# Performance work log

Hardware: AMD Instinct MI355X
Metric: run time of the kernel (lower is better)

The kernel has to match this reference:

```python
import jax, jax.numpy as jnp
import numpy as np

DIM = 512

def setup_inputs() -> dict:
    key = jax.random.key(0)
    kx, kq, kk, kv = jax.random.split(key, 4)
    x = jax.random.normal(kx, (8, 2048, DIM), dtype=jnp.float32)
    # Dense kernels are [in_dim, out_dim], no bias
    Wq = jax.random.normal(kq, (DIM, DIM), dtype=jnp.float32) * (DIM ** -0.5)
    Wk = jax.random.normal(kk, (DIM, DIM), dtype=jnp.float32) * (DIM ** -0.5)
    Wv = jax.random.normal(kv, (DIM, DIM), dtype=jnp.float32) * (DIM ** -0.5)
    return {"x": x, "Wq": Wq, "Wk": Wk, "Wv": Wv}

def reference(x, Wq, Wk, Wv):
    # x: [b, s, d]
    q = jnp.einsum('bsd,de->bse', x, Wq)
    k = jnp.einsum('bsd,de->bse', x, Wk)
    v = jnp.einsum('bsd,de->bse', x, Wv)
    scale = jnp.sqrt(jnp.asarray(DIM, dtype=x.dtype))
    attn = jnp.einsum('bqe,bke->bqk', q, k) / scale  # [b, s, s]
    attn = jax.nn.softmax(attn, axis=-1)
    return jnp.einsum('bqk,bke->bqe', attn, v)  # [b, s, d]
```

## Files before the change

kernel.cpp:

```cpp
#include <hip/hip_runtime.h>
#include <stdint.h>

typedef unsigned short u16;
typedef unsigned int u32;
typedef float floatx4 __attribute__((ext_vector_type(4)));
typedef __bf16 bf16x8 __attribute__((ext_vector_type(8)));
typedef __attribute__((address_space(1))) const u32 gu32;
typedef __attribute__((address_space(3))) u32 lu32;

#define SEQ 2048
#define DIM 512
#define NBATCH 8

#if defined(__has_builtin)
#if __has_builtin(__builtin_amdgcn_cvt_pk_bf16_f32)
#define HAVE_PK_BF16 1
#endif
#endif
#ifndef HAVE_PK_BF16
#define HAVE_PK_BF16 0
#endif

__device__ __forceinline__ u16 f2bf(float f) {
#if HAVE_PK_BF16
  auto p = __builtin_amdgcn_cvt_pk_bf16_f32(f, f);
  union { decltype(p) v; u16 u[2]; } cv; cv.v = p;
  return cv.u[0];
#else
  u32 u = __float_as_uint(f);
  u += 0x7fffu + ((u >> 16) & 1u);
  return (u16)(u >> 16);
#endif
}

__device__ __forceinline__ void stage_tile64(const u16* __restrict__ g, int ld, int k0, u16* lds) {
  const int t = threadIdx.x;
  const int wave = t >> 6, lane = t & 63;
  const int rsub = lane >> 3;
  const int lg = (lane & 7) ^ rsub;
#pragma unroll
  for (int q = 0; q < 4; ++q) {
    const int chunk = wave * 4 + q;
    const int row = chunk * 8 + rsub;
    const u16* gp = g + (size_t)row * ld + k0 + lg * 8;
    u16* lp = lds + chunk * 512 + lane * 8;
    __builtin_amdgcn_global_load_lds((gu32*)gp, (lu32*)lp, 16, 0, 0);
  }
}

__device__ __forceinline__ void gemm_core(const u16* A, const u16* BT, int lda, int ldb, int kdim,
                                          u16* As, u16* Bs, floatx4 acc[4][4]) {
  const int t = threadIdx.x;
  const int wave = t >> 6, lane = t & 63;
  const int wr = (wave >> 1) * 64, wc = (wave & 1) * 64;
  const int l15 = lane & 15, quad = lane >> 4;
  const int swz = l15 & 7;
  for (int k0 = 0; k0 < kdim; k0 += 64) {
    stage_tile64(A, lda, k0, As);
    stage_tile64(BT, ldb, k0, Bs);
    __syncthreads();
#pragma unroll
    for (int ks = 0; ks < 2; ++ks) {
      const int pg = ((ks << 2) + quad) ^ swz;
      bf16x8 af[4], bfr[4];
#pragma unroll
      for (int i = 0; i < 4; ++i) {
        af[i]  = *(const bf16x8*)(As + (wr + i * 16 + l15) * 64 + pg * 8);
        bfr[i] = *(const bf16x8*)(Bs + (wc + i * 16 + l15) * 64 + pg * 8);
      }
#pragma unroll
      for (int mi = 0; mi < 4; ++mi)
#pragma unroll
        for (int ni = 0; ni < 4; ++ni)
          acc[mi][ni] = __builtin_amdgcn_mfma_f32_16x16x32_bf16(af[mi], bfr[ni], acc[mi][ni], 0, 0, 0);
    }
    __syncthreads();
  }
}

__device__ __forceinline__ void zero_acc(floatx4 acc[4][4]) {
#pragma unroll
  for (int i = 0; i < 4; ++i)
#pragma unroll
    for (int j = 0; j < 4; ++j)
      acc[i][j] = (floatx4){0.f, 0.f, 0.f, 0.f};
}

__global__ __launch_bounds__(256) void k_prep(const float* __restrict__ x,
                                              const float* __restrict__ Wq, const float* __restrict__ Wk,
                                              const float* __restrict__ Wv,
                                              u16* __restrict__ xb, u16* __restrict__ wt) {
  __shared__ float tile[64][65];
  const int t = threadIdx.x;
  if (blockIdx.x < 4096) {
    size_t i = ((size_t)blockIdx.x * 256 + t) * 8;
    float4 a = *(const float4*)(x + i);
    float4 b = *(const float4*)(x + i + 4);
    u16 o[8] = {f2bf(a.x), f2bf(a.y), f2bf(a.z), f2bf(a.w),
                f2bf(b.x), f2bf(b.y), f2bf(b.z), f2bf(b.w)};
    *(uint4*)(xb + i) = *(const uint4*)o;
    return;
  }
  const int r = blockIdx.x - 4096;
  const int sec = r >> 6, rem = r & 63;
  const int kb = (rem & 7) * 64, nb0 = (rem >> 3) * 64;
  const float* W = (sec == 0) ? Wq : (sec == 1) ? Wk : Wv;
#pragma unroll
  for (int i = 0; i < 4; ++i) {
    int kr = i * 16 + (t >> 4), nc = (t & 15) * 4;
    float4 v = *(const float4*)&W[(size_t)(kb + kr) * 512 + nb0 + nc];
    tile[kr][nc] = v.x; tile[kr][nc + 1] = v.y; tile[kr][nc + 2] = v.z; tile[kr][nc + 3] = v.w;
  }
  __syncthreads();
#pragma unroll
  for (int i = 0; i < 4; ++i) {
    int nr = i * 16 + (t >> 4), kc = (t & 15) * 4;
    u16 o[4] = {f2bf(tile[kc][nr]), f2bf(tile[kc + 1][nr]), f2bf(tile[kc + 2][nr]), f2bf(tile[kc + 3][nr])};
    *(uint2*)&wt[(size_t)(sec * 512 + nb0 + nr) * 512 + kb + kc] = *(const uint2*)o;
  }
}

__global__ __launch_bounds__(256, 4) void k_qkv(const u16* __restrict__ xb, const u16* __restrict__ wt,
                                                u16* __restrict__ qo, u16* __restrict__ ko,
                                                u16* __restrict__ vt) {
  __shared__ __align__(16) u16 As[128 * 64];
  __shared__ __align__(16) u16 Bs[128 * 64];
  const int m0 = blockIdx.x * 128, n0 = blockIdx.y * 128;
  floatx4 acc[4][4];
  zero_acc(acc);
  gemm_core(xb + (size_t)m0 * DIM, wt + (size_t)n0 * DIM, DIM, DIM, DIM, As, Bs, acc);
  const int t = threadIdx.x, wave = t >> 6, lane = t & 63;
  const int wr = (wave >> 1) * 64, wc = (wave & 1) * 64;
  const int l15 = lane & 15, quad = lane >> 4;
  const int sec = n0 >> 9;
#pragma unroll
  for (int mi = 0; mi < 4; ++mi)
#pragma unroll
    for (int ni = 0; ni < 4; ++ni)
#pragma unroll
      for (int r = 0; r < 4; ++r) {
        int m = m0 + wr + mi * 16 + quad * 4 + r;
        int n = n0 + wc + ni * 16 + l15;
        float v = acc[mi][ni][r];
        int nc = n & 511;
        if (sec == 0) {
          qo[(size_t)m * DIM + nc] = f2bf(v * 0.04419417382415922f);
        } else if (sec == 1) {
          ko[(size_t)m * DIM + nc] = f2bf(v);
        } else {
          int b = m >> 11, s = m & 2047;
          vt[((size_t)(b * DIM + nc)) * SEQ + s] = f2bf(v);
        }
      }
}

__global__ __launch_bounds__(256, 4) void k_scores(const u16* __restrict__ q, const u16* __restrict__ kk,
                                                   u16* __restrict__ sc, float* __restrict__ rowsum,
                                                   int b0) {
  __shared__ __align__(16) u16 As[128 * 64];
  __shared__ __align__(16) u16 Bs[128 * 64];
  const int bz = blockIdx.z, bb = b0 + bz;
  const int xcd = blockIdx.x & 7, j = blockIdx.x >> 3;
  const int m0 = (j & 15) * 128, n0 = (xcd * 2 + (j >> 4)) * 128;
  floatx4 acc[4][4];
  zero_acc(acc);
  gemm_core(q + (size_t)bb * SEQ * DIM + (size_t)m0 * DIM,
            kk + (size_t)bb * SEQ * DIM + (size_t)n0 * DIM, DIM, DIM, DIM, As, Bs, acc);
  u16* C = sc + (size_t)bz * SEQ * SEQ;
  float* rsb = rowsum + (size_t)bb * SEQ;
  const int t = threadIdx.x, wave = t >> 6, lane = t & 63;
  const int wr = (wave >> 1) * 64, wc = (wave & 1) * 64;
  const int l15 = lane & 15, quad = lane >> 4;
#pragma unroll
  for (int mi = 0; mi < 4; ++mi)
#pragma unroll
    for (int r = 0; r < 4; ++r) {
      int m = m0 + wr + mi * 16 + quad * 4 + r;
      float p = 0.f;
      float ev[4];
#pragma unroll
      for (int ni = 0; ni < 4; ++ni) {
        ev[ni] = __expf(acc[mi][ni][r]);
        p += ev[ni];
      }
#pragma unroll
      for (int ni = 0; ni < 4; ++ni) {
        int n = n0 + wc + ni * 16 + l15;
        C[(size_t)m * SEQ + n] = f2bf(ev[ni]);
      }
      p += __shfl_xor(p, 1); p += __shfl_xor(p, 2);
      p += __shfl_xor(p, 4); p += __shfl_xor(p, 8);
      if (l15 == 0) atomicAdd(&rsb[m], p);
    }
}

__global__ __launch_bounds__(256, 4) void k_pv(const u16* __restrict__ sc, const u16* __restrict__ vt,
                                               const float* __restrict__ rowsum,
                                               float* __restrict__ out, int b0) {
  __shared__ __align__(16) u16 As[128 * 64];
  __shared__ __align__(16) u16 Bs[128 * 64];
  const int bz = blockIdx.z, bb = b0 + bz;
  const int xcd = blockIdx.x & 7, j = blockIdx.x >> 3;
  const int m0 = (xcd * 2 + (j & 1)) * 128, n0 = (j >> 1) * 128;
  floatx4 acc[4][4];
  zero_acc(acc);
  gemm_core(sc + (size_t)bz * SEQ * SEQ + (size_t)m0 * SEQ,
            vt + (size_t)bb * DIM * SEQ + (size_t)n0 * SEQ, SEQ, SEQ, SEQ, As, Bs, acc);
  float* C = out + (size_t)bb * SEQ * DIM;
  const float* rsb = rowsum + (size_t)bb * SEQ;
  const int t = threadIdx.x, wave = t >> 6, lane = t & 63;
  const int wr = (wave >> 1) * 64, wc = (wave & 1) * 64;
  const int l15 = lane & 15, quad = lane >> 4;
#pragma unroll
  for (int mi = 0; mi < 4; ++mi)
#pragma unroll
    for (int r = 0; r < 4; ++r) {
      int m = m0 + wr + mi * 16 + quad * 4 + r;
      float inv = 1.0f / rsb[m];
#pragma unroll
      for (int ni = 0; ni < 4; ++ni) {
        int n = n0 + wc + ni * 16 + l15;
        C[(size_t)m * DIM + n] = acc[mi][ni][r] * inv;
      }
    }
}

extern "C" void kernel_launch(void* const* d_in, const int* in_sizes, int n_in,
                              void* d_out, int out_size, void* d_ws, size_t ws_size,
                              hipStream_t stream) {
  const float* x  = (const float*)d_in[0];
  const float* Wq = (const float*)d_in[1];
  const float* Wk = (const float*)d_in[2];
  const float* Wv = (const float*)d_in[3];
  float* out = (float*)d_out;
  char* ws = (char*)d_ws;

  u16* xb   = (u16*)(ws + 0);
  u16* wt   = (u16*)(ws + 16777216);
  u16* qo   = (u16*)(ws + 18350080);
  u16* ko   = (u16*)(ws + 35127296);
  u16* vt   = (u16*)(ws + 51904512);
  float* rs = (float*)(ws + 68681728);
  u16* sc   = (u16*)(ws + 68747264);
  const size_t base_need = 68747264;
  const size_t per_b = (size_t)SEQ * SEQ * 2;
  size_t avail = (ws_size > base_need) ? (ws_size - base_need) : 0;
  int nb = (int)(avail / per_b);
  if (nb < 1) nb = 1;
  if (nb > NBATCH) nb = NBATCH;

  hipMemsetAsync(rs, 0, (size_t)NBATCH * SEQ * sizeof(float), stream);
  k_prep<<<dim3(4288), dim3(256), 0, stream>>>(x, Wq, Wk, Wv, xb, wt);
  k_qkv<<<dim3(128, 12), dim3(256), 0, stream>>>(xb, wt, qo, ko, vt);
  for (int b0 = 0; b0 < NBATCH; b0 += nb) {
    int nbr = (NBATCH - b0 < nb) ? (NBATCH - b0) : nb;
    k_scores<<<dim3(256, 1, nbr), dim3(256), 0, stream>>>(qo, ko, sc, rs, b0);
    k_pv<<<dim3(64, 1, nbr), dim3(256), 0, stream>>>(sc, vt, rs, out, b0);
  }
}
```

Measured before the change: 216.3 us.

## Double-buffer LDS staging in GEMM core and compute V^T with a separate GEMM

The shared GEMM core now double-buffers its LDS tiles, issuing the async global-to-LDS loads for the next K tile before computing the current one, and drops one barrier per iteration. The aim is to overlap memory fetches with MFMA work. V is now produced by a dedicated kernel that computes W_v^T·x^T directly, so V^T is written with coalesced rows instead of the earlier strided transposed stores. The trade-off is twice the LDS per block, which can lower occupancy below the four blocks per CU the launch bounds request.

```diff
diff --git a/kernel.cpp b/kernel.cpp
--- a/kernel.cpp
+++ b/kernel.cpp
@@ -11,6 +11,7 @@
 #define SEQ 2048
 #define DIM 512
 #define NBATCH 8
+#define TOTS (NBATCH * SEQ)
 
 #if defined(__has_builtin)
 #if __has_builtin(__builtin_amdgcn_cvt_pk_bf16_f32)
@@ -55,18 +56,26 @@
   const int wr = (wave >> 1) * 64, wc = (wave & 1) * 64;
   const int l15 = lane & 15, quad = lane >> 4;
   const int swz = l15 & 7;
+  stage_tile64(A, lda, 0, As);
+  stage_tile64(BT, ldb, 0, Bs);
+  __syncthreads();
+  int cur = 0;
   for (int k0 = 0; k0 < kdim; k0 += 64) {
-    stage_tile64(A, lda, k0, As);
-    stage_tile64(BT, ldb, k0, Bs);
-    __syncthreads();
+    const int lastiter = (k0 + 64 >= kdim);
+    if (!lastiter) {
+      stage_tile64(A, lda, k0 + 64, As + ((cur ^ 1) * (128 * 64)));
+      stage_tile64(BT, ldb, k0 + 64, Bs + ((cur ^ 1) * (128 * 64)));
+    }
+    const u16* Ac = As + cur * (128 * 64);
+    const u16* Bc = Bs + cur * (128 * 64);
 #pragma unroll
     for (int ks = 0; ks < 2; ++ks) {
       const int pg = ((ks << 2) + quad) ^ swz;
       bf16x8 af[4], bfr[4];
 #pragma unroll
       for (int i = 0; i < 4; ++i) {
-        af[i]  = *(const bf16x8*)(As + (wr + i * 16 + l15) * 64 + pg * 8);
-        bfr[i] = *(const bf16x8*)(Bs + (wc + i * 16 + l15) * 64 + pg * 8);
+        af[i]  = *(const bf16x8*)(Ac + (wr + i * 16 + l15) * 64 + pg * 8);
+        bfr[i] = *(const bf16x8*)(Bc + (wc + i * 16 + l15) * 64 + pg * 8);
       }
 #pragma unroll
       for (int mi = 0; mi < 4; ++mi)
@@ -74,7 +83,8 @@
         for (int ni = 0; ni < 4; ++ni)
           acc[mi][ni] = __builtin_amdgcn_mfma_f32_16x16x32_bf16(af[mi], bfr[ni], acc[mi][ni], 0, 0, 0);
     }
-    __syncthreads();
+    if (!lastiter) __syncthreads();
+    cur ^= 1;
   }
 }
 
@@ -121,10 +131,9 @@
 }
 
 __global__ __launch_bounds__(256, 4) void k_qkv(const u16* __restrict__ xb, const u16* __restrict__ wt,
-                                                u16* __restrict__ qo, u16* __restrict__ ko,
-                                                u16* __restrict__ vt) {
-  __shared__ __align__(16) u16 As[128 * 64];
-  __shared__ __align__(16) u16 Bs[128 * 64];
+                                                u16* __restrict__ qo, u16* __restrict__ ko) {
+  __shared__ __align__(16) u16 As[2 * 128 * 64];
+  __shared__ __align__(16) u16 Bs[2 * 128 * 64];
   const int m0 = blockIdx.x * 128, n0 = blockIdx.y * 128;
   floatx4 acc[4][4];
   zero_acc(acc);
@@ -133,6 +142,32 @@
   const int wr = (wave >> 1) * 64, wc = (wave & 1) * 64;
   const int l15 = lane & 15, quad = lane >> 4;
   const int sec = n0 >> 9;
+  u16* __restrict__ C = sec ? ko : qo;
+  const float scl = sec ? 1.0f : 0.04419417382415922f;
+#pragma unroll
+  for (int mi = 0; mi < 4; ++mi)
+#pragma unroll
+    for (int ni = 0; ni < 4; ++ni)
+#pragma unroll
+      for (int r = 0; r < 4; ++r) {
+        int m = m0 + wr + mi * 16 + quad * 4 + r;
+        int nc = (n0 + wc + ni * 16 + l15) & 511;
+        C[(size_t)m * DIM + nc] = f2bf(acc[mi][ni][r] * scl);
+      }
+}
+
+__global__ __launch_bounds__(256, 4) void k_vt(const u16* __restrict__ xb, const u16* __restrict__ wt,
+                                               u16* __restrict__ vt) {
+  __shared__ __align__(16) u16 As[2 * 128 * 64];
+  __shared__ __align__(16) u16 Bs[2 * 128 * 64];
+  const int m0 = blockIdx.x * 128;
+  const int n0 = blockIdx.y * 128;
+  floatx4 acc[4][4];
+  zero_acc(acc);
+  gemm_core(wt + (size_t)(2 * DIM + m0) * DIM, xb + (size_t)n0 * DIM, DIM, DIM, DIM, As, Bs, acc);
+  const int t = threadIdx.x, wave = t >> 6, lane = t & 63;
+  const int wr = (wave >> 1) * 64, wc = (wave & 1) * 64;
+  const int l15 = lane & 15, quad = lane >> 4;
 #pragma unroll
   for (int mi = 0; mi < 4; ++mi)
 #pragma unroll
@@ -141,24 +176,15 @@
       for (int r = 0; r < 4; ++r) {
         int m = m0 + wr + mi * 16 + quad * 4 + r;
         int n = n0 + wc + ni * 16 + l15;
-        float v = acc[mi][ni][r];
-        int nc = n & 511;
-        if (sec == 0) {
-          qo[(size_t)m * DIM + nc] = f2bf(v * 0.04419417382415922f);
-        } else if (sec == 1) {
-          ko[(size_t)m * DIM + nc] = f2bf(v);
-        } else {
-          int b = m >> 11, s = m & 2047;
-          vt[((size_t)(b * DIM + nc)) * SEQ + s] = f2bf(v);
-        }
+        vt[(size_t)m * TOTS + n] = f2bf(acc[mi][ni][r]);
       }
 }
 
 __global__ __launch_bounds__(256, 4) void k_scores(const u16* __restrict__ q, const u16* __restrict__ kk,
                                                    u16* __restrict__ sc, float* __restrict__ rowsum,
                                                    int b0) {
-  __shared__ __align__(16) u16 As[128 * 64];
-  __shared__ __align__(16) u16 Bs[128 * 64];
+  __shared__ __align__(16) u16 As[2 * 128 * 64];
+  __shared__ __align__(16) u16 Bs[2 * 128 * 64];
   const int bz = blockIdx.z, bb = b0 + bz;
   const int xcd = blockIdx.x & 7, j = blockIdx.x >> 3;
   const int m0 = (j & 15) * 128, n0 = (xcd * 2 + (j >> 4)) * 128;
@@ -197,15 +223,15 @@
 __global__ __launch_bounds__(256, 4) void k_pv(const u16* __restrict__ sc, const u16* __restrict__ vt,
                                                const float* __restrict__ rowsum,
                                                float* __restrict__ out, int b0) {
-  __shared__ __align__(16) u16 As[128 * 64];
-  __shared__ __align__(16) u16 Bs[128 * 64];
+  __shared__ __align__(16) u16 As[2 * 128 * 64];
+  __shared__ __align__(16) u16 Bs[2 * 128 * 64];
   const int bz = blockIdx.z, bb = b0 + bz;
   const int xcd = blockIdx.x & 7, j = blockIdx.x >> 3;
   const int m0 = (xcd * 2 + (j & 1)) * 128, n0 = (j >> 1) * 128;
   floatx4 acc[4][4];
   zero_acc(acc);
   gemm_core(sc + (size_t)bz * SEQ * SEQ + (size_t)m0 * SEQ,
-            vt + (size_t)bb * DIM * SEQ + (size_t)n0 * SEQ, SEQ, SEQ, SEQ, As, Bs, acc);
+            vt + (size_t)n0 * TOTS + (size_t)bb * SEQ, SEQ, TOTS, SEQ, As, Bs, acc);
   float* C = out + (size_t)bb * SEQ * DIM;
   const float* rsb = rowsum + (size_t)bb * SEQ;
   const int t = threadIdx.x, wave = t >> 6, lane = t & 63;
@@ -251,7 +277,8 @@
 
   hipMemsetAsync(rs, 0, (size_t)NBATCH * SEQ * sizeof(float), stream);
   k_prep<<<dim3(4288), dim3(256), 0, stream>>>(x, Wq, Wk, Wv, xb, wt);
-  k_qkv<<<dim3(128, 12), dim3(256), 0, stream>>>(xb, wt, qo, ko, vt);
+  k_qkv<<<dim3(128, 8), dim3(256), 0, stream>>>(xb, wt, qo, ko);
+  k_vt<<<dim3(4, 128), dim3(256), 0, stream>>>(xb, wt, vt);
   for (int b0 = 0; b0 < NBATCH; b0 += nb) {
     int nbr = (NBATCH - b0 < nb) ? (NBATCH - b0) : nb;
     k_scores<<<dim3(256, 1, nbr), dim3(256), 0, stream>>>(qo, ko, sc, rs, b0);
```

Result: slower. 229.7 us (+6.2%).

## Use 3-stage LDS ring pipeline with 256x128 tiles and 8-wave blocks

Applied to the files above, without the earlier changes.

Replaces the synchronous stage-then-compute GEMM loop with a three-slot LDS ring that prefetches two k-steps ahead using vmcnt waits and a single barrier per step. Blocks grow to 512 threads covering 256x128 output tiles, which halves the grid sizes. The V projection is recomputed as a transposed GEMM (W^T times x) so V^T is written with coalesced stores instead of strided scatter. This is meant to hide global-load latency and improve operand reuse, at the cost of much larger LDS use per block (144 KB), fewer resident blocks and fewer blocks to fill the CUs.

```diff
diff --git a/kernel.cpp b/kernel.cpp
--- a/kernel.cpp
+++ b/kernel.cpp
@@ -11,6 +11,7 @@
 #define SEQ 2048
 #define DIM 512
 #define NBATCH 8
+#define TOTS (NBATCH * SEQ)
 
 #if defined(__has_builtin)
 #if __has_builtin(__builtin_amdgcn_cvt_pk_bf16_f32)
@@ -33,7 +34,8 @@
 #endif
 }
 
-__device__ __forceinline__ void stage_tile64(const u16* __restrict__ g, int ld, int k0, u16* lds) {
+
+__device__ __forceinline__ void stageA(const u16* __restrict__ g, int ld, int k0, u16* lds) {
   const int t = threadIdx.x;
   const int wave = t >> 6, lane = t & 63;
   const int rsub = lane >> 3;
@@ -48,25 +50,55 @@
   }
 }
 
-__device__ __forceinline__ void gemm_core(const u16* A, const u16* BT, int lda, int ldb, int kdim,
+__device__ __forceinline__ void stageB(const u16* __restrict__ g, int ld, int k0, u16* lds) {
+  const int t = threadIdx.x;
+  const int wave = t >> 6, lane = t & 63;
+  const int rsub = lane >> 3;
+  const int lg = (lane & 7) ^ rsub;
+#pragma unroll
+  for (int q = 0; q < 2; ++q) {
+    const int chunk = wave * 2 + q;
+    const int row = chunk * 8 + rsub;
+    const u16* gp = g + (size_t)row * ld + k0 + lg * 8;
+    u16* lp = lds + chunk * 512 + lane * 8;
+    __builtin_amdgcn_global_load_lds((gu32*)gp, (lu32*)lp, 16, 0, 0);
+  }
+}
+
+__device__ __forceinline__ void gemm_ring(const u16* __restrict__ A, int lda,
+                                          const u16* __restrict__ BT, int ldb, int kdim,
                                           u16* As, u16* Bs, floatx4 acc[4][4]) {
   const int t = threadIdx.x;
-  const int wave = t >> 6, lane = t & 63;
-  const int wr = (wave >> 1) * 64, wc = (wave & 1) * 64;
+  const int w = t >> 6, lane = t & 63;
+  const int wm = w & 3, wn = w >> 2;
   const int l15 = lane & 15, quad = lane >> 4;
   const int swz = l15 & 7;
-  for (int k0 = 0; k0 < kdim; k0 += 64) {
-    stage_tile64(A, lda, k0, As);
-    stage_tile64(BT, ldb, k0, Bs);
-    __syncthreads();
+  const int nsteps = kdim >> 6;
+
+  stageA(A, lda, 0, As);           stageB(BT, ldb, 0, Bs);
+  stageA(A, lda, 64, As + 16384);  stageB(BT, ldb, 64, Bs + 8192);
+
+  int slot = 0;
+  for (int kt = 0; kt < nsteps; ++kt) {
+    if (kt + 1 < nsteps) asm volatile("s_waitcnt vmcnt(6)" ::: "memory");
+    else                 asm volatile("s_waitcnt vmcnt(0)" ::: "memory");
+    __builtin_amdgcn_s_barrier();
+    asm volatile("" ::: "memory");
+    if (kt + 2 < nsteps) {
+      int ss = slot + 2; if (ss >= 3) ss -= 3;
+      stageA(A, lda, (kt + 2) << 6, As + ss * 16384);
+      stageB(BT, ldb, (kt + 2) << 6, Bs + ss * 8192);
+    }
+    const u16* Ac = As + slot * 16384;
+    const u16* Bc = Bs + slot * 8192;
 #pragma unroll
     for (int ks = 0; ks < 2; ++ks) {
       const int pg = ((ks << 2) + quad) ^ swz;
       bf16x8 af[4], bfr[4];
 #pragma unroll
       for (int i = 0; i < 4; ++i) {
-        af[i]  = *(const bf16x8*)(As + (wr + i * 16 + l15) * 64 + pg * 8);
-        bfr[i] = *(const bf16x8*)(Bs + (wc + i * 16 + l15) * 64 + pg * 8);
+        af[i]  = *(const bf16x8*)(Ac + (wm * 64 + i * 16 + l15) * 64 + pg * 8);
+        bfr[i] = *(const bf16x8*)(Bc + (wn * 64 + i * 16 + l15) * 64 + pg * 8);
       }
 #pragma unroll
       for (int mi = 0; mi < 4; ++mi)
@@ -74,7 +106,7 @@
         for (int ni = 0; ni < 4; ++ni)
           acc[mi][ni] = __builtin_amdgcn_mfma_f32_16x16x32_bf16(af[mi], bfr[ni], acc[mi][ni], 0, 0, 0);
     }
-    __syncthreads();
+    ++slot; if (slot == 3) slot = 0;
   }
 }
 
@@ -120,62 +152,74 @@
   }
 }
 
-__global__ __launch_bounds__(256, 4) void k_qkv(const u16* __restrict__ xb, const u16* __restrict__ wt,
-                                                u16* __restrict__ qo, u16* __restrict__ ko,
-                                                u16* __restrict__ vt) {
-  __shared__ __align__(16) u16 As[128 * 64];
-  __shared__ __align__(16) u16 Bs[128 * 64];
-  const int m0 = blockIdx.x * 128, n0 = blockIdx.y * 128;
+__global__ __launch_bounds__(512, 2) void k_proj(const u16* __restrict__ xb, const u16* __restrict__ wt,
+                                                 u16* __restrict__ qo, u16* __restrict__ ko,
+                                                 u16* __restrict__ vt) {
+  __shared__ __align__(16) u16 As[3 * 256 * 64];
+  __shared__ __align__(16) u16 Bs[3 * 128 * 64];
+  const int gx = blockIdx.x;
   floatx4 acc[4][4];
   zero_acc(acc);
-  gemm_core(xb + (size_t)m0 * DIM, wt + (size_t)n0 * DIM, DIM, DIM, DIM, As, Bs, acc);
-  const int t = threadIdx.x, wave = t >> 6, lane = t & 63;
-  const int wr = (wave >> 1) * 64, wc = (wave & 1) * 64;
+  const int t = threadIdx.x, w = t >> 6, lane = t & 63;
+  const int wm = w & 3, wn = w >> 2;
   const int l15 = lane & 15, quad = lane >> 4;
-  const int sec = n0 >> 9;
-#pragma unroll
-  for (int mi = 0; mi < 4; ++mi)
-#pragma unroll
-    for (int ni = 0; ni < 4; ++ni)
-#pragma unroll
-      for (int r = 0; r < 4; ++r) {
-        int m = m0 + wr + mi * 16 + quad * 4 + r;
-        int n = n0 + wc + ni * 16 + l15;
-        float v = acc[mi][ni][r];
-        int nc = n & 511;
-        if (sec == 0) {
-          qo[(size_t)m * DIM + nc] = f2bf(v * 0.04419417382415922f);
-        } else if (sec == 1) {
-          ko[(size_t)m * DIM + nc] = f2bf(v);
-        } else {
-          int b = m >> 11, s = m & 2047;
-          vt[((size_t)(b * DIM + nc)) * SEQ + s] = f2bf(v);
+  if (gx < 512) {
+    const int m0 = (gx & 63) * 256, n0 = (gx >> 6) * 128;
+    gemm_ring(xb + (size_t)m0 * DIM, DIM, wt + (size_t)n0 * DIM, DIM, DIM, As, Bs, acc);
+    const int sec = n0 >> 9;
+    u16* __restrict__ C = sec ? ko : qo;
+    const float scl = sec ? 1.0f : 0.04419417382415922f;
+#pragma unroll
+    for (int mi = 0; mi < 4; ++mi)
+#pragma unroll
+      for (int ni = 0; ni < 4; ++ni)
+#pragma unroll
+        for (int r = 0; r < 4; ++r) {
+          int m = m0 + wm * 64 + mi * 16 + quad * 4 + r;
+          int nc = (n0 + wn * 64 + ni * 16 + l15) & 511;
+          C[(size_t)m * DIM + nc] = f2bf(acc[mi][ni][r] * scl);
         }
-      }
-}
-
-__global__ __launch_bounds__(256, 4) void k_scores(const u16* __restrict__ q, const u16* __restrict__ kk,
+  } else {
+    const int rr = gx - 512;
+    const int m0 = (rr & 1) * 256;
+    const int n0 = (rr >> 1) * 128;
+    gemm_ring(wt + (size_t)(2 * DIM + m0) * DIM, DIM, xb + (size_t)n0 * DIM, DIM, DIM, As, Bs, acc);
+#pragma unroll
+    for (int mi = 0; mi < 4; ++mi)
+#pragma unroll
+      for (int ni = 0; ni < 4; ++ni)
+#pragma unroll
+        for (int r = 0; r < 4; ++r) {
+          int m = m0 + wm * 64 + mi * 16 + quad * 4 + r;
+          int n = n0 + wn * 64 + ni * 16 + l15;
+          vt[(size_t)m * TOTS + n] = f2bf(acc[mi][ni][r]);
+        }
+  }
+}
+
+__global__ __launch_bounds__(512, 2) void k_scores(const u16* __restrict__ q, const u16* __restrict__ kk,
                                                    u16* __restrict__ sc, float* __restrict__ rowsum,
                                                    int b0) {
-  __shared__ __align__(16) u16 As[128 * 64];
-  __shared__ __align__(16) u16 Bs[128 * 64];
+  __shared__ __align__(16) u16 As[3 * 256 * 64];
+  __shared__ __align__(16) u16 Bs[3 * 128 * 64];
   const int bz = blockIdx.z, bb = b0 + bz;
   const int xcd = blockIdx.x & 7, j = blockIdx.x >> 3;
-  const int m0 = (j & 15) * 128, n0 = (xcd * 2 + (j >> 4)) * 128;
+  const int n0 = (xcd * 2 + (j & 1)) * 128;
+  const int m0 = (j >> 1) * 256;
   floatx4 acc[4][4];
   zero_acc(acc);
-  gemm_core(q + (size_t)bb * SEQ * DIM + (size_t)m0 * DIM,
-            kk + (size_t)bb * SEQ * DIM + (size_t)n0 * DIM, DIM, DIM, DIM, As, Bs, acc);
+  gemm_ring(q + (size_t)bb * SEQ * DIM + (size_t)m0 * DIM, DIM,
+            kk + (size_t)bb * SEQ * DIM + (size_t)n0 * DIM, DIM, DIM, As, Bs, acc);
   u16* C = sc + (size_t)bz * SEQ * SEQ;
   float* rsb = rowsum + (size_t)bb * SEQ;
-  const int t = threadIdx.x, wave = t >> 6, lane = t & 63;
-  const int wr = (wave >> 1) * 64, wc = (wave & 1) * 64;
+  const int t = threadIdx.x, w = t >> 6, lane = t & 63;
+  const int wm = w & 3, wn = w >> 2;
   const int l15 = lane & 15, quad = lane >> 4;
 #pragma unroll
   for (int mi = 0; mi < 4; ++mi)
 #pragma unroll
     for (int r = 0; r < 4; ++r) {
-      int m = m0 + wr + mi * 16 + quad * 4 + r;
+      int m = m0 + wm * 64 + mi * 16 + quad * 4 + r;
       float p = 0.f;
       float ev[4];
 #pragma unroll
@@ -185,7 +229,7 @@
       }
 #pragma unroll
       for (int ni = 0; ni < 4; ++ni) {
-        int n = n0 + wc + ni * 16 + l15;
+        int n = n0 + wn * 64 + ni * 16 + l15;
         C[(size_t)m * SEQ + n] = f2bf(ev[ni]);
       }
       p += __shfl_xor(p, 1); p += __shfl_xor(p, 2);
@@ -194,32 +238,32 @@
     }
 }
 
-__global__ __launch_bounds__(256, 4) void k_pv(const u16* __restrict__ sc, const u16* __restrict__ vt,
+__global__ __launch_bounds__(512, 2) void k_pv(const u16* __restrict__ sc, const u16* __restrict__ vt,
                                                const float* __restrict__ rowsum,
                                                float* __restrict__ out, int b0) {
-  __shared__ __align__(16) u16 As[128 * 64];
-  __shared__ __align__(16) u16 Bs[128 * 64];
+  __shared__ __align__(16) u16 As[3 * 256 * 64];
+  __shared__ __align__(16) u16 Bs[3 * 128 * 64];
   const int bz = blockIdx.z, bb = b0 + bz;
   const int xcd = blockIdx.x & 7, j = blockIdx.x >> 3;
-  const int m0 = (xcd * 2 + (j & 1)) * 128, n0 = (j >> 1) * 128;
+  const int m0 = xcd * 256, n0 = j * 128;
   floatx4 acc[4][4];
   zero_acc(acc);
-  gemm_core(sc + (size_t)bz * SEQ * SEQ + (size_t)m0 * SEQ,
-            vt + (size_t)bb * DIM * SEQ + (size_t)n0 * SEQ, SEQ, SEQ, SEQ, As, Bs, acc);
+  gemm_ring(sc + (size_t)bz * SEQ * SEQ + (size_t)m0 * SEQ, SEQ,
+            vt + (size_t)n0 * TOTS + (size_t)bb * SEQ, TOTS, SEQ, As, Bs, acc);
   float* C = out + (size_t)bb * SEQ * DIM;
   const float* rsb = rowsum + (size_t)bb * SEQ;
-  const int t = threadIdx.x, wave = t >> 6, lane = t & 63;
-  const int wr = (wave >> 1) * 64, wc = (wave & 1) * 64;
+  const int t = threadIdx.x, w = t >> 6, lane = t & 63;
+  const int wm = w & 3, wn = w >> 2;
   const int l15 = lane & 15, quad = lane >> 4;
 #pragma unroll
   for (int mi = 0; mi < 4; ++mi)
 #pragma unroll
     for (int r = 0; r < 4; ++r) {
-      int m = m0 + wr + mi * 16 + quad * 4 + r;
+      int m = m0 + wm * 64 + mi * 16 + quad * 4 + r;
       float inv = 1.0f / rsb[m];
 #pragma unroll
       for (int ni = 0; ni < 4; ++ni) {
-        int n = n0 + wc + ni * 16 + l15;
+        int n = n0 + wn * 64 + ni * 16 + l15;
         C[(size_t)m * DIM + n] = acc[mi][ni][r] * inv;
       }
     }
@@ -251,10 +295,10 @@
 
   hipMemsetAsync(rs, 0, (size_t)NBATCH * SEQ * sizeof(float), stream);
   k_prep<<<dim3(4288), dim3(256), 0, stream>>>(x, Wq, Wk, Wv, xb, wt);
-  k_qkv<<<dim3(128, 12), dim3(256), 0, stream>>>(xb, wt, qo, ko, vt);
+  k_proj<<<dim3(768), dim3(512), 0, stream>>>(xb, wt, qo, ko, vt);
   for (int b0 = 0; b0 < NBATCH; b0 += nb) {
     int nbr = (NBATCH - b0 < nb) ? (NBATCH - b0) : nb;
-    k_scores<<<dim3(256, 1, nbr), dim3(256), 0, stream>>>(qo, ko, sc, rs, b0);
-    k_pv<<<dim3(64, 1, nbr), dim3(256), 0, stream>>>(sc, vt, rs, out, b0);
-  }
-}
+    k_scores<<<dim3(128, 1, nbr), dim3(512), 0, stream>>>(qo, ko, sc, rs, b0);
+    k_pv<<<dim3(32, 1, nbr), dim3(512), 0, stream>>>(sc, vt, rs, out, b0);
+  }
+}
```

New measurement: 234.1 us. +8.2%, slower.
